# Optimization experiments

Measured on AMD Instinct MI355X. Metric: run time of the kernel, lower is better.

## Reference

```python
import jax, jax.numpy as jnp
import numpy as np

E, S, L = 32, 64, 32          # episodes, steps, max_comm_len
H, D_IN, C = 512, 1536, 64    # hidden_size, pvrnn_mtrnn_size + 2*hidden, comm_shape


def setup_inputs() -> dict:
    key = jax.random.key(0)
    ks = jax.random.split(key, 12)
    sd = 0.02
    inp = {
        "h_w_action": jax.random.normal(ks[0], (E, S, D_IN), jnp.float32),
        "Wx": jax.random.normal(ks[1], (D_IN, H), jnp.float32) * sd,
        "bx": jnp.zeros((H,), jnp.float32),
        "Wh": jax.random.normal(ks[2], (H, H), jnp.float32) * sd,
        "bh": jnp.zeros((H,), jnp.float32),
        "prelu_a": jnp.float32(0.25),  # nn.PReLU default single-param init
        "Wout": jax.random.normal(ks[3], (H, C), jnp.float32) * sd,
        "bout": jnp.zeros((C,), jnp.float32),
    }
    for i, k in enumerate([1, 3, 5, 7]):
        inp[f"conv_w{k}"] = jax.random.normal(ks[4 + i], (H // 4, H, k), jnp.float32) * sd
        inp[f"conv_b{k}"] = jnp.zeros((H // 4,), jnp.float32)
    return inp


def _conv1d_reflect(x, w, b):
    # x: (N, Cin, L), w: (Cout, Cin, K) -> 'same' conv with reflect padding
    k = w.shape[-1]
    p = (k - 1) // 2
    if p > 0:
        x = jnp.pad(x, ((0, 0), (0, 0), (p, p)), mode="reflect")
    y = jax.lax.conv_general_dilated(
        x, w, window_strides=(1,), padding="VALID",
        dimension_numbers=("NCW", "OIW", "NCW"))
    return y + b[None, :, None]


def _forward(h_w_action, Wx, bx, Wh, bh,
             conv_w1, conv_b1, conv_w3, conv_b3,
             conv_w5, conv_b5, conv_w7, conv_b7,
             prelu_a, Wout, bout):
    e, s, d = h_w_action.shape
    x = h_w_action.reshape(e * s, d)                 # (N, D_IN)
    xw = x @ Wx + bx                                  # precompute input drive once

    # MTRNN with time_constant=1 -> h_new = tanh(Wx x + Wh h); same x every step
    def step(h, _):
        h = jnp.tanh(xw + h @ Wh + bh)
        return h, h

    h0 = jnp.zeros((e * s, H), h_w_action.dtype)
    _, hs = jax.lax.scan(step, h0, None, length=L)   # (L, N, H)
    comm_h = jnp.transpose(hs, (1, 2, 0))            # (N, H, L) channels-first

    # Ted_Conv1d: 4 parallel convs (kernels 1,3,5,7), concat on channels
    y = jnp.concatenate([
        _conv1d_reflect(comm_h, conv_w1, conv_b1),
        _conv1d_reflect(comm_h, conv_w3, conv_b3),
        _conv1d_reflect(comm_h, conv_w5, conv_b5),
        _conv1d_reflect(comm_h, conv_w7, conv_b7),
    ], axis=1)                                        # (N, H, L)
    y = jnp.where(y >= 0, y, prelu_a * y)             # PReLU; dropout is eval-mode identity

    y = jnp.transpose(y, (0, 2, 1)).reshape(e, s, L, H)
    comm_pred = y @ Wout + bout                       # (E, S, L, C)

    # create_comm_mask: keep tokens up to and including the first end token (argmax == 0)
    is_end = jnp.argmax(comm_pred, axis=-1) == 0      # (E, S, L)
    before_first_end = (jnp.cumsum(is_end.astype(jnp.int32), axis=-1)
                        - is_end.astype(jnp.int32)) == 0
    mask = before_first_end.astype(comm_pred.dtype)
    return comm_pred * mask[..., None]


def reference(h_w_action, Wx, bx, Wh, bh,
              conv_w1, conv_b1, conv_w3, conv_b3,
              conv_w5, conv_b5, conv_w7, conv_b7,
              prelu_a, Wout, bout):
    return _forward(h_w_action, Wx, bx, Wh, bh,
                    conv_w1, conv_b1, conv_w3, conv_b3,
                    conv_w5, conv_b5, conv_w7, conv_b7,
                    prelu_a, Wout, bout)
```

## Files before the change

### kernel.cpp

```cpp
#include <hip/hip_runtime.h>
#include <cmath>

#define LSEQ 32
#define HID  512
#define DIN  1536
#define CCH  64
#define NROW 2048
#define NL   65536

typedef _Float16 f16;
typedef _Float16 f16x8 __attribute__((ext_vector_type(8)));
typedef float    f32x4 __attribute__((ext_vector_type(4)));
typedef unsigned long long u64;

__device__ __forceinline__ float fast_tanh(float x) {
  float e = __expf(2.0f * x);
  return 1.0f - 2.0f * __builtin_amdgcn_rcpf(e + 1.0f);
}

__device__ __forceinline__ int offA(int r, int b) {
  return (r << 6) + (b ^ (((r >> 1) & 3) << 4));
}
__device__ __forceinline__ int offB(int r, int b) {
  return (r << 10) + (b ^ ((r & 7) << 4));
}

__global__ void pack_wc_kernel(const float* __restrict__ w1, const float* __restrict__ w3,
                               const float* __restrict__ w5, const float* __restrict__ w7,
                               f16* __restrict__ Wc_t) {
  int idx = blockIdx.x * 256 + threadIdx.x;
  if (idx >= 7 * 512 * 512) return;
  int k   = idx & 511;
  int c   = (idx >> 9) & 511;
  int dli = idx >> 18;
  int dl  = dli - 3;
  int g   = c >> 7, cg = c & 127;
  int K   = 2 * g + 1;
  int kk  = dl + g;
  float v = 0.f;
  if (kk >= 0 && kk < K) {
    const float* w = (g == 0) ? w1 : (g == 1) ? w3 : (g == 2) ? w5 : w7;
    v = w[(cg * 512 + k) * K + kk];
  }
  Wc_t[idx] = (f16)v;
}

__global__ void pack_misc_kernel(const float* __restrict__ Wh, const float* __restrict__ Wout,
                                 const float* __restrict__ Wx,
                                 f16* __restrict__ Wh_t, f16* __restrict__ Wout_t,
                                 f16* __restrict__ Wx_t) {
  int idx = blockIdx.x * 256 + threadIdx.x;
  if (idx < 512 * 512) {
    int n = idx >> 9, k = idx & 511;
    Wh_t[idx] = (f16)Wh[k * 512 + n];
  } else if (idx < 512 * 512 + 64 * 512) {
    int j = idx - 512 * 512;
    int c = j >> 9, k = j & 511;
    Wout_t[j] = (f16)Wout[k * 64 + c];
  } else {
    int j = idx - (512 * 512 + 64 * 512);
    if (j < 512 * 1536) {
      int n = j / 1536, k = j - n * 1536;
      Wx_t[j] = (f16)Wx[k * 512 + n];
    }
  }
}

__global__ void pack_x_kernel(const float* __restrict__ x,
                              f16* __restrict__ x_hi, f16* __restrict__ x_lo) {
  int idx = blockIdx.x * 256 + threadIdx.x;
  float v = x[idx];
  f16 hi = (f16)v;
  x_hi[idx] = hi;
  x_lo[idx] = (f16)(v - (float)hi);
}

__global__ __launch_bounds__(256) void xw_mfma_kernel(
    const f16* __restrict__ x_hi, const f16* __restrict__ x_lo,
    const f16* __restrict__ Wx_t, const float* __restrict__ bx,
    float* __restrict__ xw)
{
  __shared__ __align__(16) char Ah[2][4096], Al[2][4096], Bt[2][8192];
  const int tid = threadIdx.x, lane = tid & 63, wave = tid >> 6;
  const int r0 = blockIdx.x * 64, c0 = blockIdx.y * 128;
  const int wr = (wave >> 1) * 32, wc = (wave & 1) * 64;
  const int q = lane >> 4, ln = lane & 15, qb = q << 4;

  const int arow = tid & 63, acb = (tid >> 6) << 4;
  const char* srcAh = (const char*)(x_hi + (size_t)(r0 + arow) * DIN) + acb;
  const char* srcAl = (const char*)(x_lo + (size_t)(r0 + arow) * DIN) + acb;
  const int wAo = offA(arow, acb);
  const int brow = tid & 127, bcb = (tid >> 7) << 5;
  const char* srcB = (const char*)(Wx_t + (size_t)(c0 + brow) * DIN) + bcb;
  const int wB0 = offA(brow, bcb), wB1 = offA(brow, bcb + 16);

  *(int4*)(Ah[0] + wAo) = *(const int4*)(srcAh);
  *(int4*)(Al[0] + wAo) = *(const int4*)(srcAl);
  *(int4*)(Bt[0] + wB0) = *(const int4*)(srcB);
  *(int4*)(Bt[0] + wB1) = *(const int4*)(srcB + 16);
  __syncthreads();

  f32x4 acc[2][4] = {};
  for (int kk = 0; kk < 48; ++kk) {
    const int buf = kk & 1;
    int4 ra, rl, rb0, rb1;
    if (kk < 47) {
      ra  = *(const int4*)(srcAh + (kk + 1) * 64);
      rl  = *(const int4*)(srcAl + (kk + 1) * 64);
      rb0 = *(const int4*)(srcB  + (kk + 1) * 64);
      rb1 = *(const int4*)(srcB  + (kk + 1) * 64 + 16);
    }
    f16x8 bf[4];
#pragma unroll
    for (int n = 0; n < 4; ++n)
      bf[n] = *(const f16x8*)(Bt[buf] + offA(wc + n * 16 + ln, qb));
#pragma unroll
    for (int m = 0; m < 2; ++m) {
      f16x8 ah = *(const f16x8*)(Ah[buf] + offA(wr + m * 16 + ln, qb));
      f16x8 al = *(const f16x8*)(Al[buf] + offA(wr + m * 16 + ln, qb));
#pragma unroll
      for (int n = 0; n < 4; ++n) {
        acc[m][n] = __builtin_amdgcn_mfma_f32_16x16x32_f16(ah, bf[n], acc[m][n], 0, 0, 0);
        acc[m][n] = __builtin_amdgcn_mfma_f32_16x16x32_f16(al, bf[n], acc[m][n], 0, 0, 0);
      }
    }
    if (kk < 47) {
      *(int4*)(Ah[buf ^ 1] + wAo) = ra;
      *(int4*)(Al[buf ^ 1] + wAo) = rl;
      *(int4*)(Bt[buf ^ 1] + wB0) = rb0;
      *(int4*)(Bt[buf ^ 1] + wB1) = rb1;
      __syncthreads();
    }
  }
#pragma unroll
  for (int m = 0; m < 2; ++m)
#pragma unroll
    for (int i = 0; i < 4; ++i) {
      const int R = r0 + wr + m * 16 + q * 4 + i;
#pragma unroll
      for (int n = 0; n < 4; ++n) {
        const int C = c0 + wc + n * 16 + ln;
        xw[(size_t)R * HID + C] = acc[m][n][i] + bx[C];
      }
    }
}

__global__ __launch_bounds__(1024, 4) void rnn_all_kernel(
    f16* __restrict__ hs_hi, const f16* __restrict__ Wh_t,
    const float* __restrict__ xw, const float* __restrict__ bh)
{
  __shared__ __align__(16) char Hs[2][2][16384];
  const int tid = threadIdx.x, lane = tid & 63, w = tid >> 6;
  const int n0 = blockIdx.x * 16;
  const int q = lane >> 4, ln = lane & 15;

  float xwbh[2][4];
  {
    const float* xwrow = xw + (size_t)(n0 + ln) * HID + w * 32 + (q << 2);
    const float* bhp   = bh + w * 32 + (q << 2);
#pragma unroll
    for (int nt = 0; nt < 2; ++nt) {
      float4 xv = *(const float4*)(xwrow + nt * 16);
      float4 bv = *(const float4*)(bhp + nt * 16);
      xwbh[nt][0] = xv.x + bv.x;
      xwbh[nt][1] = xv.y + bv.y;
      xwbh[nt][2] = xv.z + bv.z;
      xwbh[nt][3] = xv.w + bv.w;
    }
  }

  const char* pA0 = (const char*)Wh_t + ((size_t)(w * 32 + ln) << 10) + (q << 4);
  const char* pA1 = pA0 + (16 << 10);

  f16x8 wh0[16];
#pragma unroll
  for (int ks = 0; ks < 16; ++ks)
    wh0[ks] = *(const f16x8*)(pA0 + (ks << 6));

  int wo[2];
#pragma unroll
  for (int nt = 0; nt < 2; ++nt) {
    const int sub = nt * 2 + (q >> 1);
    wo[nt] = (w << 10) | (sub << 8) | ((ln ^ (w & 7)) << 4) | ((q & 1) << 3);
  }
  const int cks = lane >> 2;
  const int cpySrc = (cks << 10) | ((lane & 3) << 8) | ((w ^ (cks & 7)) << 4);
  char* gdst = (char*)hs_hi + (((size_t)(n0 + w) * LSEQ) << 10) + (lane << 4);

  for (int ts = 0; ts < LSEQ; ++ts) {
    f32x4 acc0 = {}, acc1 = {};
    if (ts > 0) {
      const char* Hb = Hs[(ts - 1) & 1][0];
      f16x8 a1c = *(const f16x8*)(pA1);
#pragma unroll
      for (int ks = 0; ks < 16; ++ks) {
        f16x8 a1 = a1c;
        if (ks < 15) a1c = *(const f16x8*)(pA1 + ((ks + 1) << 6));
        const int ro = (ks << 10) | ((lane ^ (ks & 7)) << 4);
        f16x8 bhf = *(const f16x8*)(Hb + ro);
        f16x8 blf = *(const f16x8*)(Hb + 16384 + ro);
        acc0 = __builtin_amdgcn_mfma_f32_16x16x32_f16(wh0[ks], bhf, acc0, 0, 0, 0);
        acc0 = __builtin_amdgcn_mfma_f32_16x16x32_f16(wh0[ks], blf, acc0, 0, 0, 0);
        acc1 = __builtin_amdgcn_mfma_f32_16x16x32_f16(a1, bhf, acc1, 0, 0, 0);
        acc1 = __builtin_amdgcn_mfma_f32_16x16x32_f16(a1, blf, acc1, 0, 0, 0);
      }
    }
    char* Hw = Hs[ts & 1][0];
#pragma unroll
    for (int nt = 0; nt < 2; ++nt) {
      f32x4 ac = nt ? acc1 : acc0;
      union { u64 u; f16 h[4]; } H, L;
#pragma unroll
      for (int i = 0; i < 4; ++i) {
        float v = fast_tanh(ac[i] + xwbh[nt][i]);
        f16 hi = (f16)v;
        H.h[i] = hi;
        L.h[i] = (f16)(v - (float)hi);
      }
      *(u64*)(Hw + wo[nt])         = H.u;
      *(u64*)(Hw + 16384 + wo[nt]) = L.u;
    }
    __syncthreads();
    *(int4*)(gdst + (ts << 10)) = *(const int4*)(Hw + cpySrc);
  }
}

__global__ __launch_bounds__(256) void conv_mfma_kernel(
    const f16* __restrict__ hs_hi, const f16* __restrict__ Wc_t,
    const float* __restrict__ b1, const float* __restrict__ b3,
    const float* __restrict__ b5, const float* __restrict__ b7,
    const float* __restrict__ prelu_a, f16* __restrict__ y)
{
  __shared__ __align__(16) char Atile[2][8192];
  __shared__ __align__(16) char Btile[2][8192];
  const int tid = threadIdx.x, lane = tid & 63, wave = tid >> 6;
  const int r0 = blockIdx.x * 128;
  const int g  = blockIdx.y;
  const int taps = 2 * g + 1;
  const int wr = (wave >> 1) * 64, wc = (wave & 1) * 64;
  const int q = lane >> 4, ln = lane & 15;

  const int srow = tid >> 1;
  const int sb   = (tid & 1) << 5;
  const char* srcA = (const char*)(hs_hi + (size_t)(r0 + srow) * HID) + sb;
  const int wA0 = offA(srow, sb), wA1 = offA(srow, sb + 16);

  *(int4*)(Atile[0] + wA0) = *(const int4*)(srcA);
  *(int4*)(Atile[0] + wA1) = *(const int4*)(srcA + 16);
  {
    const char* p = (const char*)(Wc_t + ((size_t)(0 - g + 3) * HID + (g * 128 + srow)) * HID) + sb;
    *(int4*)(Btile[0] + wA0) = *(const int4*)(p);
    *(int4*)(Btile[0] + wA1) = *(const int4*)(p + 16);
  }
  __syncthreads();

  f32x4 acc[4][4] = {};
  int cur = 0, curA = 0;
  for (int kk = 0; kk < 16; ++kk) {
    for (int tp = 0; tp < taps; ++tp) {
      const bool lastPhase = (kk == 15) && (tp == taps - 1);
      const int nkk = (tp == taps - 1) ? kk + 1 : kk;
      const int ntp = (tp == taps - 1) ? 0 : tp + 1;
      int4 rb0, rb1, ra0, ra1;
      bool stA = false;
      if (!lastPhase) {
        const char* p = (const char*)(Wc_t + ((size_t)(ntp - g + 3) * HID + (g * 128 + srow)) * HID + nkk * 32) + sb;
        rb0 = *(const int4*)(p);
        rb1 = *(const int4*)(p + 16);
        if (ntp == 0) {
          stA = true;
          ra0 = *(const int4*)(srcA + nkk * 64);
          ra1 = *(const int4*)(srcA + nkk * 64 + 16);
        }
      }
      const int dl = tp - g;
      f16x8 af[4], bf[4];
#pragma unroll
      for (int m = 0; m < 4; ++m) {
        const int lr = wr + m * 16 + ln;
        int tt = (lr & 31) + dl;
        tt = (tt < 0) ? -tt : ((tt > 31) ? 62 - tt : tt);
        af[m] = *(const f16x8*)(Atile[curA] + offA((lr & ~31) | tt, q << 4));
      }
#pragma unroll
      for (int n = 0; n < 4; ++n)
        bf[n] = *(const f16x8*)(Btile[cur] + offA(wc + n * 16 + ln, q << 4));
      __builtin_amdgcn_s_setprio(1);
#pragma unroll
      for (int m = 0; m < 4; ++m)
#pragma unroll
        for (int n = 0; n < 4; ++n)
          acc[m][n] = __builtin_amdgcn_mfma_f32_16x16x32_f16(af[m], bf[n], acc[m][n], 0, 0, 0);
      __builtin_amdgcn_s_setprio(0);
      if (!lastPhase) {
        *(int4*)(Btile[cur ^ 1] + wA0) = rb0;
        *(int4*)(Btile[cur ^ 1] + wA1) = rb1;
        if (stA) {
          *(int4*)(Atile[curA ^ 1] + wA0) = ra0;
          *(int4*)(Atile[curA ^ 1] + wA1) = ra1;
        }
        __syncthreads();
        cur ^= 1;
        if (stA) curA ^= 1;
      }
    }
  }

  const float pa = *prelu_a;
  const float* bg = (g == 0) ? b1 : (g == 1) ? b3 : (g == 2) ? b5 : b7;
#pragma unroll
  for (int m = 0; m < 4; ++m)
#pragma unroll
    for (int i = 0; i < 4; ++i) {
      const int R = r0 + wr + m * 16 + q * 4 + i;
#pragma unroll
      for (int n = 0; n < 4; ++n) {
        const int cg = wc + n * 16 + ln;
        float v = acc[m][n][i] + bg[cg];
        v = (v >= 0.f) ? v : pa * v;
        y[(size_t)R * HID + g * 128 + cg] = (f16)v;
      }
    }
}

__global__ __launch_bounds__(256) void out_mfma_kernel(
    const f16* __restrict__ y, const f16* __restrict__ Wout_t,
    const float* __restrict__ bout, float* __restrict__ out)
{
  __shared__ __align__(16) char Bl[65536];
  __shared__ __align__(16) char Atile[2][8192];
  const int tid = threadIdx.x, lane = tid & 63, wave = tid >> 6;
  const int r0 = blockIdx.x * 128;
  const int q = lane >> 4, ln = lane & 15;

  {
    const int rr = tid >> 2;
    const char* src = (const char*)(Wout_t + (size_t)rr * HID);
#pragma unroll
    for (int i = 0; i < 16; ++i) {
      const int cb = (((tid & 3) + (i << 2)) << 4);
      *(int4*)(Bl + offB(rr, cb)) = *(const int4*)(src + cb);
    }
  }
  const int srow = tid >> 1, sb = (tid & 1) << 5;
  const char* srcA = (const char*)(y + (size_t)(r0 + srow) * HID) + sb;
  const int wA0 = offA(srow, sb), wA1 = offA(srow, sb + 16);
  *(int4*)(Atile[0] + wA0) = *(const int4*)(srcA);
  *(int4*)(Atile[0] + wA1) = *(const int4*)(srcA + 16);
  __syncthreads();

  f32x4 acc[2][4] = {};
#pragma unroll
  for (int ks = 0; ks < 16; ++ks) {
    const int buf = ks & 1;
    int4 na0, na1;
    if (ks < 15) {
      na0 = *(const int4*)(srcA + (ks + 1) * 64);
      na1 = *(const int4*)(srcA + (ks + 1) * 64 + 16);
    }
    f16x8 af[2], bf[4];
#pragma unroll
    for (int m = 0; m < 2; ++m)
      af[m] = *(const f16x8*)(Atile[buf] + offA(wave * 32 + m * 16 + ln, q << 4));
#pragma unroll
    for (int n = 0; n < 4; ++n)
      bf[n] = *(const f16x8*)(Bl + offB(n * 16 + ln, (ks << 6) + (q << 4)));
#pragma unroll
    for (int m = 0; m < 2; ++m)
#pragma unroll
      for (int n = 0; n < 4; ++n)
        acc[m][n] = __builtin_amdgcn_mfma_f32_16x16x32_f16(af[m], bf[n], acc[m][n], 0, 0, 0);
    if (ks < 15) {
      *(int4*)(Atile[buf ^ 1] + wA0) = na0;
      *(int4*)(Atile[buf ^ 1] + wA1) = na1;
      __syncthreads();
    }
  }
#pragma unroll
  for (int m = 0; m < 2; ++m)
#pragma unroll
    for (int i = 0; i < 4; ++i) {
      const int R = r0 + wave * 32 + m * 16 + q * 4 + i;
#pragma unroll
      for (int n = 0; n < 4; ++n) {
        const int C = n * 16 + ln;
        out[(size_t)R * CCH + C] = acc[m][n][i] + bout[C];
      }
    }
}

__global__ void mask_kernel(float* __restrict__ out) {
  const int row  = blockIdx.x;
  const int lane = threadIdx.x;
  float* base = out + (long)row * (LSEQ * CCH);
  int ended = 0;
  for (int l = 0; l < LSEQ; ++l) {
    float v = base[l * CCH + lane];
    float mv = v; int mi = lane;
#pragma unroll
    for (int off = 32; off > 0; off >>= 1) {
      float ov = __shfl_xor(mv, off);
      int   oi = __shfl_xor(mi, off);
      if (ov > mv || (ov == mv && oi < mi)) { mv = ov; mi = oi; }
    }
    if (ended) base[l * CCH + lane] = 0.f;
    ended |= (mi == 0);
  }
}

extern "C" void kernel_launch(void* const* d_in, const int* in_sizes, int n_in,
                              void* d_out, int out_size, void* d_ws, size_t ws_size,
                              hipStream_t stream) {
  const float* x    = (const float*)d_in[0];
  const float* Wx   = (const float*)d_in[1];
  const float* bx   = (const float*)d_in[2];
  const float* Wh   = (const float*)d_in[3];
  const float* bh   = (const float*)d_in[4];
  const float* pa   = (const float*)d_in[5];
  const float* Wout = (const float*)d_in[6];
  const float* bout = (const float*)d_in[7];
  const float* cw1  = (const float*)d_in[8];
  const float* cb1  = (const float*)d_in[9];
  const float* cw3  = (const float*)d_in[10];
  const float* cb3  = (const float*)d_in[11];
  const float* cw5  = (const float*)d_in[12];
  const float* cb5  = (const float*)d_in[13];
  const float* cw7  = (const float*)d_in[14];
  const float* cb7  = (const float*)d_in[15];
  float* out = (float*)d_out;

  char* ws = (char*)d_ws;
  f16*   hs_hi  = (f16*)(ws);
  f16*   Wout_t = (f16*)(ws + 67108864);
  f16*   Wc_t   = (f16*)(ws + 67174400);
  char*  big    = ws + 70844416;
  float* xw     = (float*)(big);
  f16*   Wh_t   = (f16*)(big + 4194304);
  f16*   x_hi   = (f16*)(big + 4718592);
  f16*   x_lo   = (f16*)(big + 11010048);
  f16*   Wx_t   = (f16*)(big + 17301504);
  f16*   y      = (f16*)(big);

  pack_wc_kernel<<<7 * 512 * 512 / 256, 256, 0, stream>>>(cw1, cw3, cw5, cw7, Wc_t);
  pack_misc_kernel<<<4224, 256, 0, stream>>>(Wh, Wout, Wx, Wh_t, Wout_t, Wx_t);
  pack_x_kernel<<<NROW * DIN / 256, 256, 0, stream>>>(x, x_hi, x_lo);

  xw_mfma_kernel<<<dim3(NROW / 64, HID / 128), 256, 0, stream>>>(x_hi, x_lo, Wx_t, bx, xw);

  rnn_all_kernel<<<NROW / 16, 1024, 0, stream>>>(hs_hi, Wh_t, xw, bh);

  conv_mfma_kernel<<<dim3(NL / 128, 4), 256, 0, stream>>>(
      hs_hi, Wc_t, cb1, cb3, cb5, cb7, pa, y);

  out_mfma_kernel<<<NL / 128, 256, 0, stream>>>(y, Wout_t, bout, out);

  mask_kernel<<<NROW, 64, 0, stream>>>(out);
}
```

Baseline: 436.4 us.

## Halve RNN block to 8 waves, each holding 64 columns of Wh in registers

The recurrent kernel now runs 512 threads per block instead of 1024. Each wave computes four 16-column tiles instead of two and keeps all four tiles of Wh resident in registers, so the per-step global reload of half of Wh goes away. Each B fragment read from LDS now feeds four MFMA tiles, which cuts LDS traffic per MFMA and reduces barrier participants. In exchange, register pressure rises sharply (256 VGPRs of weights alone), which may force spills, and there are fewer waves per CU to hide latency.

```diff
diff --git a/kernel.cpp b/kernel.cpp
--- a/kernel.cpp
+++ b/kernel.cpp
@@ -145,7 +145,7 @@
     }
 }
 
-__global__ __launch_bounds__(1024, 4) void rnn_all_kernel(
+__global__ __launch_bounds__(512, 2) void rnn_all_kernel(
     f16* __restrict__ hs_hi, const f16* __restrict__ Wh_t,
     const float* __restrict__ xw, const float* __restrict__ bh)
 {
@@ -153,13 +153,14 @@
   const int tid = threadIdx.x, lane = tid & 63, w = tid >> 6;
   const int n0 = blockIdx.x * 16;
   const int q = lane >> 4, ln = lane & 15;
-
-  float xwbh[2][4];
+  const int cbase = w * 64;
+
+  float xwbh[4][4];
   {
-    const float* xwrow = xw + (size_t)(n0 + ln) * HID + w * 32 + (q << 2);
-    const float* bhp   = bh + w * 32 + (q << 2);
-#pragma unroll
-    for (int nt = 0; nt < 2; ++nt) {
+    const float* xwrow = xw + (size_t)(n0 + ln) * HID + cbase + (q << 2);
+    const float* bhp   = bh + cbase + (q << 2);
+#pragma unroll
+    for (int nt = 0; nt < 4; ++nt) {
       float4 xv = *(const float4*)(xwrow + nt * 16);
       float4 bv = *(const float4*)(bhp + nt * 16);
       xwbh[nt][0] = xv.x + bv.x;
@@ -169,50 +170,52 @@
     }
   }
 
-  const char* pA0 = (const char*)Wh_t + ((size_t)(w * 32 + ln) << 10) + (q << 4);
-  const char* pA1 = pA0 + (16 << 10);
-
-  f16x8 wh0[16];
-#pragma unroll
-  for (int ks = 0; ks < 16; ++ks)
-    wh0[ks] = *(const f16x8*)(pA0 + (ks << 6));
-
-  int wo[2];
-#pragma unroll
-  for (int nt = 0; nt < 2; ++nt) {
-    const int sub = nt * 2 + (q >> 1);
-    wo[nt] = (w << 10) | (sub << 8) | ((ln ^ (w & 7)) << 4) | ((q & 1) << 3);
-  }
+  f16x8 wh[4][16];
+#pragma unroll
+  for (int nt = 0; nt < 4; ++nt) {
+    const char* pA = (const char*)Wh_t + ((size_t)(cbase + nt * 16 + ln) << 10) + (q << 4);
+#pragma unroll
+    for (int ks = 0; ks < 16; ++ks)
+      wh[nt][ks] = *(const f16x8*)(pA + (ks << 6));
+  }
+
+  int wo[4];
+#pragma unroll
+  for (int nt = 0; nt < 4; ++nt) {
+    const int ksp  = w * 2 + (nt >> 1);
+    const int kgrp = ((nt & 1) << 1) | (q >> 1);
+    wo[nt] = (ksp << 10) | (kgrp << 8) | ((ln ^ (ksp & 7)) << 4) | ((q & 1) << 3);
+  }
+
   const int cks = lane >> 2;
-  const int cpySrc = (cks << 10) | ((lane & 3) << 8) | ((w ^ (cks & 7)) << 4);
-  char* gdst = (char*)hs_hi + (((size_t)(n0 + w) * LSEQ) << 10) + (lane << 4);
+  const int src0 = (cks << 10) | ((lane & 3) << 8) | ((w ^ (cks & 7)) << 4);
+  const int src1 = (cks << 10) | ((lane & 3) << 8) | (((w + 8) ^ (cks & 7)) << 4);
+  char* gdst0 = (char*)hs_hi + (((size_t)(n0 + w) * LSEQ) << 10) + (lane << 4);
+  char* gdst1 = (char*)hs_hi + (((size_t)(n0 + w + 8) * LSEQ) << 10) + (lane << 4);
 
   for (int ts = 0; ts < LSEQ; ++ts) {
-    f32x4 acc0 = {}, acc1 = {};
+    f32x4 acc[4] = {};
     if (ts > 0) {
       const char* Hb = Hs[(ts - 1) & 1][0];
-      f16x8 a1c = *(const f16x8*)(pA1);
 #pragma unroll
       for (int ks = 0; ks < 16; ++ks) {
-        f16x8 a1 = a1c;
-        if (ks < 15) a1c = *(const f16x8*)(pA1 + ((ks + 1) << 6));
         const int ro = (ks << 10) | ((lane ^ (ks & 7)) << 4);
         f16x8 bhf = *(const f16x8*)(Hb + ro);
         f16x8 blf = *(const f16x8*)(Hb + 16384 + ro);
-        acc0 = __builtin_amdgcn_mfma_f32_16x16x32_f16(wh0[ks], bhf, acc0, 0, 0, 0);
-        acc0 = __builtin_amdgcn_mfma_f32_16x16x32_f16(wh0[ks], blf, acc0, 0, 0, 0);
-        acc1 = __builtin_amdgcn_mfma_f32_16x16x32_f16(a1, bhf, acc1, 0, 0, 0);
-        acc1 = __builtin_amdgcn_mfma_f32_16x16x32_f16(a1, blf, acc1, 0, 0, 0);
+#pragma unroll
+        for (int nt = 0; nt < 4; ++nt) {
+          acc[nt] = __builtin_amdgcn_mfma_f32_16x16x32_f16(wh[nt][ks], bhf, acc[nt], 0, 0, 0);
+          acc[nt] = __builtin_amdgcn_mfma_f32_16x16x32_f16(wh[nt][ks], blf, acc[nt], 0, 0, 0);
+        }
       }
     }
     char* Hw = Hs[ts & 1][0];
 #pragma unroll
-    for (int nt = 0; nt < 2; ++nt) {
-      f32x4 ac = nt ? acc1 : acc0;
+    for (int nt = 0; nt < 4; ++nt) {
       union { u64 u; f16 h[4]; } H, L;
 #pragma unroll
       for (int i = 0; i < 4; ++i) {
-        float v = fast_tanh(ac[i] + xwbh[nt][i]);
+        float v = fast_tanh(acc[nt][i] + xwbh[nt][i]);
         f16 hi = (f16)v;
         H.h[i] = hi;
         L.h[i] = (f16)(v - (float)hi);
@@ -221,7 +224,8 @@
       *(u64*)(Hw + 16384 + wo[nt]) = L.u;
     }
     __syncthreads();
-    *(int4*)(gdst + (ts << 10)) = *(const int4*)(Hw + cpySrc);
+    *(int4*)(gdst0 + (ts << 10)) = *(const int4*)(Hw + src0);
+    *(int4*)(gdst1 + (ts << 10)) = *(const int4*)(Hw + src1);
   }
 }
 
@@ -447,7 +451,7 @@
 
   xw_mfma_kernel<<<dim3(NROW / 64, HID / 128), 256, 0, stream>>>(x_hi, x_lo, Wx_t, bx, xw);
 
-  rnn_all_kernel<<<NROW / 16, 1024, 0, stream>>>(hs_hi, Wh_t, xw, bh);
+  rnn_all_kernel<<<NROW / 16, 512, 0, stream>>>(hs_hi, Wh_t, xw, bh);
 
   conv_mfma_kernel<<<dim3(NL / 128, 4), 256, 0, stream>>>(
       hs_hi, Wc_t, cb1, cb3, cb5, cb7, pa, y);
```

After: 441.1 us. About the same (+1.1%).
